# Performance work log

Measured on AMD Instinct MI355X. Metric: run time of the kernel, lower is better.

The kernel has to match this reference:

```python
import jax, jax.numpy as jnp
from jax import lax
import numpy as np

B, IMG, P, CIN, D, DEPTH, H, FF = 32, 512, 16, 4, 256, 4, 8, 2048
N = (IMG // P) ** 2          # 1024 patches
L = N // 2                   # exactly 512 masked patches per batch (static max_len)
DH = D // H
EPS = 1e-5


def layer_norm(x, s, b):
    m = x.mean(-1, keepdims=True)
    v = ((x - m) ** 2).mean(-1, keepdims=True)
    return (x - m) * lax.rsqrt(v + EPS) * s + b


def setup_inputs() -> dict:
    key = jax.random.key(0)
    ks = jax.random.split(key, 16)
    init = lambda k, shp: 0.02 * jax.random.normal(k, shp, jnp.float32)

    image = jax.random.normal(ks[0], (B, 3, IMG, IMG), jnp.float32)
    # patch-granular binary mask: exactly L patches per batch have value 0 (masked)
    scores = jax.random.uniform(ks[1], (B, N))
    idx = jnp.argsort(scores, axis=1)[:, :L]
    pm = jnp.ones((B, N), jnp.float32).at[jnp.arange(B)[:, None], idx].set(0.0)
    mask = jnp.repeat(jnp.repeat(pm.reshape(B, 1, IMG // P, IMG // P), P, 2), P, 3)

    return dict(
        image=image, mask=mask,
        conv_w=init(ks[2], (D, CIN, P, P)), conv_b=jnp.zeros((D,), jnp.float32),
        pos_embed=jax.random.normal(ks[3], (1, N, D), jnp.float32),
        qkv_w=init(ks[4], (DEPTH, D, 3 * D)), qkv_b=jnp.zeros((DEPTH, 3 * D), jnp.float32),
        out_w=init(ks[5], (DEPTH, D, D)), out_b=jnp.zeros((DEPTH, D), jnp.float32),
        ln1_s=jnp.ones((DEPTH, D), jnp.float32), ln1_b=jnp.zeros((DEPTH, D), jnp.float32),
        ff1_w=init(ks[6], (DEPTH, D, FF)), ff1_b=jnp.zeros((DEPTH, FF), jnp.float32),
        ff2_w=init(ks[7], (DEPTH, FF, D)), ff2_b=jnp.zeros((DEPTH, D), jnp.float32),
        ln2_s=jnp.ones((DEPTH, D), jnp.float32), ln2_b=jnp.zeros((DEPTH, D), jnp.float32),
    )


def reference(image, mask, conv_w, conv_b, pos_embed, qkv_w, qkv_b, out_w, out_b,
              ln1_s, ln1_b, ff1_w, ff1_b, ff2_w, ff2_b, ln2_s, ln2_b):
    xin = jnp.concatenate([image, mask], axis=1)                       # [B,4,512,512]
    x = lax.conv_general_dilated(xin, conv_w, (P, P), 'VALID',
                                 dimension_numbers=('NCHW', 'OIHW', 'NCHW'))
    x = x + conv_b[None, :, None, None]                                # [B,D,32,32]
    Bc = x.shape[0]
    x = x.reshape(Bc, D, N).transpose(0, 2, 1)                         # [B,N,D]

    # nearest downsample (factor exactly P): sample at indices i*P
    pmask = mask[:, 0, ::P, ::P].reshape(Bc, N)
    sel = pmask < 0.5                                                  # masked patches
    # stable compaction: indices of masked patches first, in original order
    order = jnp.argsort(jnp.logical_not(sel), axis=1, stable=True)[:, :L]
    tokens = jnp.take_along_axis(x, order[..., None], axis=1)          # [B,L,D]
    pos = pos_embed[0][order]                                          # [B,L,D]
    lengths = sel.sum(axis=1)
    valid = (jnp.arange(L)[None, :] < lengths[:, None])[..., None]
    h = jnp.where(valid, tokens + pos, 0.0)                            # zero padding

    scale = 1.0 / np.sqrt(DH)
    for i in range(DEPTH):  # post-norm torch TransformerEncoderLayer, no dropout
        qkv = h @ qkv_w[i] + qkv_b[i]
        q, k, v = jnp.split(qkv, 3, axis=-1)
        q = q.reshape(Bc, L, H, DH)
        k = k.reshape(Bc, L, H, DH)
        v = v.reshape(Bc, L, H, DH)
        att = jax.nn.softmax(jnp.einsum('bqhd,bkhd->bhqk', q, k) * scale, axis=-1)
        o = jnp.einsum('bhqk,bkhd->bqhd', att, v).reshape(Bc, L, D)
        h = layer_norm(h + o @ out_w[i] + out_b[i], ln1_s[i], ln1_b[i])
        ff = jax.nn.relu(h @ ff1_w[i] + ff1_b[i]) @ ff2_w[i] + ff2_b[i]
        h = layer_norm(h + ff, ln2_s[i], ln2_b[i])
    return h
```

## Files before the change

kernel.cpp:

```cpp
#include <hip/hip_runtime.h>
#include <cstdint>
#include <cstddef>


#define Bq 32
#define Dm 256
#define Lq 512
#define Hh 8
#define FFq 2048
#define Mtok (Bq * Lq)

typedef __attribute__((ext_vector_type(8))) short  short8;
typedef __attribute__((ext_vector_type(4))) float  f32x4;
typedef __attribute__((ext_vector_type(4))) unsigned int u32x4;
typedef __attribute__((ext_vector_type(2))) unsigned int u32x2;

static __device__ __forceinline__ unsigned short f2bf(float f) {
    unsigned int u = __float_as_uint(f);
    unsigned int r = (u + 0x7FFFu + ((u >> 16) & 1u)) >> 16;
    return (unsigned short)r;
}
static __device__ __forceinline__ unsigned int pk2bf(float lo, float hi) {
    return (unsigned int)f2bf(lo) | ((unsigned int)f2bf(hi) << 16);
}

static __device__ __forceinline__ void gload_lds16(const void* g, void* l) {
    __builtin_amdgcn_global_load_lds(
        (const __attribute__((address_space(1))) unsigned int*)g,
        (__attribute__((address_space(3))) unsigned int*)l, 16, 0, 0);
}

static __device__ __forceinline__ int xcd_swz(int id, int grid) {
    return (id & 7) * (grid >> 3) + (id >> 3);
}

__global__ __launch_bounds__(1024) void k_order(const float* __restrict__ mask,
                                                int* __restrict__ order) {
    const int b = blockIdx.x;
    const int n = threadIdx.x;
    const float v = mask[(size_t)b * 262144 + (size_t)(n >> 5) * 8192 + (n & 31) * 16];
    const bool sel = v < 0.5f;
    const unsigned long long ball = __ballot(sel);
    const int wave = n >> 6, lane = n & 63;
    __shared__ int wsum[16];
    __shared__ int wpre[16];
    if (lane == 0) wsum[wave] = __popcll(ball);
    __syncthreads();
    if (n == 0) {
        int s = 0;
        for (int i = 0; i < 16; ++i) { wpre[i] = s; s += wsum[i]; }
    }
    __syncthreads();
    const int rank = wpre[wave] + __popcll(ball & ((1ull << lane) - 1ull));
    if (sel) order[b * Lq + rank] = n;
}

__global__ __launch_bounds__(256) void k_gather(const float* __restrict__ image,
                                                const int* __restrict__ order,
                                                const float* __restrict__ pos,
                                                unsigned short* __restrict__ patchA,
                                                float* __restrict__ posG) {
    __shared__ int pn[16];
    const int tid = threadIdx.x;
    const int tok0 = blockIdx.x * 16;
    if (tid < 16) pn[tid] = order[tok0 + tid];
    __syncthreads();
    const int lane = tid & 63, w4 = tid >> 6;
    const int rr = lane >> 2, col4 = (lane & 3) << 2;
#pragma unroll
    for (int it = 0; it < 12; ++it) {
        const int s = it * 4 + w4;
        const int t = s / 3, cch = s % 3;
        const int n = pn[t];
        const int b = (tok0 + t) >> 9;
        const int pi = n >> 5, pj = n & 31;
        const float4 v = *(const float4*)&image[
            (((size_t)b * 3 + cch) * 512 + pi * 16 + rr) * 512 + pj * 16 + col4];
        unsigned int pk[2] = {pk2bf(v.x, v.y), pk2bf(v.z, v.w)};
        *(uint2*)&patchA[(size_t)(tok0 + t) * 768 + cch * 256 + rr * 16 + col4] =
            *(uint2*)pk;
    }
#pragma unroll
    for (int it = 0; it < 4; ++it) {
        const int t = it * 4 + w4;
        *(float4*)&posG[(size_t)(tok0 + t) * Dm + lane * 4] =
            *(const float4*)&pos[(size_t)pn[t] * Dm + lane * 4];
    }
}

__global__ __launch_bounds__(256) void k_wprep_all(const float* __restrict__ qkv_w,
                                                   const float* __restrict__ out_w,
                                                   const float* __restrict__ ff1_w,
                                                   const float* __restrict__ ff2_w,
                                                   const float* __restrict__ conv_w,
                                                   unsigned short* __restrict__ Wq,
                                                   unsigned short* __restrict__ Wo,
                                                   unsigned short* __restrict__ Wf1,
                                                   unsigned short* __restrict__ Wf2,
                                                   unsigned short* __restrict__ We) {
    int idx = blockIdx.x;
    if (idx >= 1280) {
        const int i = (idx - 1280) * 256 + threadIdx.x;
        const int d = i / 96, k8 = (i % 96) * 8;
        const float4 a = *(const float4*)&conv_w[(size_t)d * 1024 + k8];
        const float4 b = *(const float4*)&conv_w[(size_t)d * 1024 + k8 + 4];
        unsigned int pk[4] = {pk2bf(a.x, a.y), pk2bf(a.z, a.w),
                              pk2bf(b.x, b.y), pk2bf(b.z, b.w)};
        *(uint4*)&We[(size_t)d * 768 + k8] = *(uint4*)pk;
        return;
    }
    __shared__ float tile[64][65];
    const float* W; unsigned short* WT; int K, N, l, r;
    if (idx < 192)      { l = idx / 48;          r = idx % 48;  K = 256;  N = 768;  W = qkv_w; WT = Wq; }
    else if (idx < 256) { l = (idx - 192) / 16;  r = idx & 15;  K = 256;  N = 256;  W = out_w; WT = Wo; }
    else if (idx < 768) { l = (idx - 256) / 128; r = (idx - 256) % 128; K = 256;  N = 2048; W = ff1_w; WT = Wf1; }
    else                { l = (idx - 768) / 128; r = (idx - 768) % 128; K = 2048; N = 256;  W = ff2_w; WT = Wf2; }
    const int nTiles = N >> 6;
    const int n0 = (r % nTiles) * 64, k0 = (r / nTiles) * 64;
    W  += (size_t)l * K * N;
    WT += (size_t)l * K * N;
    const int t = threadIdx.x;
#pragma unroll
    for (int it = 0; it < 4; ++it) {
        const int rr = (t >> 4) + it * 16, c4 = (t & 15) * 4;
        *(float4*)&tile[rr][c4] = *(const float4*)&W[(size_t)(k0 + rr) * N + n0 + c4];
    }
    __syncthreads();
    const int n = t & 63, kq = t >> 6;
    unsigned short pk[16];
#pragma unroll
    for (int j = 0; j < 16; ++j) pk[j] = f2bf(tile[kq * 16 + j][n]);
    unsigned short* dst = &WT[(size_t)(n0 + n) * K + k0 + kq * 16];
    *(uint4*)dst       = *(uint4*)&pk[0];
    *(uint4*)(dst + 8) = *(uint4*)&pk[8];
}

template <bool RELU, bool RES, bool OUT32, bool OUT16, int NBUF, bool SWZ>
__global__ __launch_bounds__(256) void k_mgemm(const unsigned short* __restrict__ A,
                                               const unsigned short* __restrict__ W,
                                               const float* __restrict__ bias,
                                               const float* __restrict__ R,
                                               float* __restrict__ C32,
                                               unsigned short* __restrict__ C16,
                                               int ntiles, int M, int N, int K) {
    __shared__ unsigned short Al[128 * 64 * NBUF];
    __shared__ unsigned short Bl[128 * 64 * NBUF];
    const int tid = threadIdx.x;
    const int lane = tid & 63, wave = tid >> 6;
    const int wm = wave >> 1, wn = wave & 1;
    int id = blockIdx.x;
    if constexpr (SWZ) id = xcd_swz(id, (int)gridDim.x);
    const int n0 = (id % ntiles) * 128, m0 = (id / ntiles) * 128;
    const int c = lane >> 4, a15 = lane & 15;
    f32x4 acc[4][4] = {};

    const int srow = lane >> 3;
    const int sgran = (lane & 7) ^ srow;
    const int KT = K >> 6;

    auto stage = [&](int buf, int kt) {
        const int k0 = kt << 6;
#pragma unroll
        for (int q = 0; q < 4; ++q) {
            const int rbase = wave * 32 + q * 8;
            gload_lds16(A + (size_t)(m0 + rbase + srow) * K + k0 + sgran * 8,
                        &Al[buf * 8192 + rbase * 64]);
            gload_lds16(W + (size_t)(n0 + rbase + srow) * K + k0 + sgran * 8,
                        &Bl[buf * 8192 + rbase * 64]);
        }
    };
    auto compute = [&](int buf) {
        const int bo = buf * 8192;
#pragma unroll
        for (int kc = 0; kc < 2; ++kc) {
            short8 af[4], bf[4];
#pragma unroll
            for (int fm = 0; fm < 4; ++fm) {
                const int row = wm * 64 + fm * 16 + a15;
                const int slot = (kc * 4 + c) ^ (row & 7);
                af[fm] = *(const short8*)&Al[bo + row * 64 + slot * 8];
            }
#pragma unroll
            for (int fn = 0; fn < 4; ++fn) {
                const int row = wn * 64 + fn * 16 + a15;
                const int slot = (kc * 4 + c) ^ (row & 7);
                bf[fn] = *(const short8*)&Bl[bo + row * 64 + slot * 8];
            }
#pragma unroll
            for (int fm = 0; fm < 4; ++fm)
#pragma unroll
                for (int fn = 0; fn < 4; ++fn)
                    acc[fm][fn] = __builtin_amdgcn_mfma_f32_16x16x32_bf16(
                        af[fm], bf[fn], acc[fm][fn], 0, 0, 0);
        }
    };

    if constexpr (NBUF == 2) {
        stage(0, 0);
        for (int kt = 0; kt < KT; ++kt) {
            const int cur = kt & 1;
            if (kt + 1 < KT) {
                stage(cur ^ 1, kt + 1);
                asm volatile("s_waitcnt vmcnt(8)" ::: "memory");
            } else {
                asm volatile("s_waitcnt vmcnt(0)" ::: "memory");
            }
            __builtin_amdgcn_s_barrier();
            compute(cur);
            __builtin_amdgcn_s_barrier();
        }
    } else {
        for (int kt = 0; kt < KT; ++kt) {
            __syncthreads();
            stage(0, kt);
            __syncthreads();
            compute(0);
        }
    }
#pragma unroll
    for (int fn = 0; fn < 4; ++fn) {
        const int col = n0 + wn * 64 + fn * 16 + a15;
        const float bv = bias[col];
#pragma unroll
        for (int fm = 0; fm < 4; ++fm) {
            const int mrow = m0 + wm * 64 + fm * 16 + c * 4;
#pragma unroll
            for (int r = 0; r < 4; ++r) {
                float v = acc[fm][fn][r] + bv;
                if constexpr (RES) v += R[(size_t)(mrow + r) * N + col];
                if constexpr (RELU) v = fmaxf(v, 0.f);
                if constexpr (OUT32) C32[(size_t)(mrow + r) * N + col] = v;
                if constexpr (OUT16) C16[(size_t)(mrow + r) * N + col] = f2bf(v);
            }
        }
    }
}

template <bool RELU, bool OUT16>
__global__ __launch_bounds__(512) void k_mgemm8(const unsigned short* __restrict__ A,
                                                const unsigned short* __restrict__ W,
                                                const float* __restrict__ bias,
                                                unsigned short* __restrict__ C16,
                                                int ntiles, int N, int K) {
    __shared__ unsigned short Al[256 * 64];
    __shared__ unsigned short Bl[128 * 64];
    const int tid = threadIdx.x;
    const int lane = tid & 63, wave = tid >> 6;
    const int wm = wave >> 1, wn = wave & 1;
    const int id = xcd_swz((int)blockIdx.x, (int)gridDim.x);
    const int n0 = (id % ntiles) * 128, m0 = (id / ntiles) * 256;
    const int c = lane >> 4, a15 = lane & 15;
    f32x4 acc[4][4] = {};

    const int srow = lane >> 3;
    const int sgran = (lane & 7) ^ srow;
    const int KT = K >> 6;

    for (int kt = 0; kt < KT; ++kt) {
        const int k0 = kt << 6;
        __syncthreads();
#pragma unroll
        for (int q = 0; q < 4; ++q) {
            const int rbase = wave * 32 + q * 8;
            gload_lds16(A + (size_t)(m0 + rbase + srow) * K + k0 + sgran * 8,
                        &Al[rbase * 64]);
        }
#pragma unroll
        for (int q = 0; q < 2; ++q) {
            const int rbase = wave * 16 + q * 8;
            gload_lds16(W + (size_t)(n0 + rbase + srow) * K + k0 + sgran * 8,
                        &Bl[rbase * 64]);
        }
        __syncthreads();
#pragma unroll
        for (int kc = 0; kc < 2; ++kc) {
            short8 af[4], bf[4];
#pragma unroll
            for (int fm = 0; fm < 4; ++fm) {
                const int row = wm * 64 + fm * 16 + a15;
                const int slot = (kc * 4 + c) ^ (row & 7);
                af[fm] = *(const short8*)&Al[row * 64 + slot * 8];
            }
#pragma unroll
            for (int fn = 0; fn < 4; ++fn) {
                const int row = wn * 64 + fn * 16 + a15;
                const int slot = (kc * 4 + c) ^ (row & 7);
                bf[fn] = *(const short8*)&Bl[row * 64 + slot * 8];
            }
#pragma unroll
            for (int fm = 0; fm < 4; ++fm)
#pragma unroll
                for (int fn = 0; fn < 4; ++fn)
                    acc[fm][fn] = __builtin_amdgcn_mfma_f32_16x16x32_bf16(
                        af[fm], bf[fn], acc[fm][fn], 0, 0, 0);
        }
    }
#pragma unroll
    for (int fn = 0; fn < 4; ++fn) {
        const int col = n0 + wn * 64 + fn * 16 + a15;
        const float bv = bias[col];
#pragma unroll
        for (int fm = 0; fm < 4; ++fm) {
            const int mrow = m0 + wm * 64 + fm * 16 + c * 4;
#pragma unroll
            for (int r = 0; r < 4; ++r) {
                float v = acc[fm][fn][r] + bv;
                if constexpr (RELU) v = fmaxf(v, 0.f);
                if constexpr (OUT16) C16[(size_t)(mrow + r) * N + col] = f2bf(v);
            }
        }
    }
}

__global__ __launch_bounds__(256) void k_gemm_ln(const unsigned short* __restrict__ A,
                                                 const unsigned short* __restrict__ W,
                                                 const float* __restrict__ bias,
                                                 const float* __restrict__ R,
                                                 const float* __restrict__ lns,
                                                 const float* __restrict__ lnb,
                                                 float* __restrict__ Y32,
                                                 unsigned short* __restrict__ Y16,
                                                 int K) {
    __shared__ unsigned short Al[32 * 64 * 2];
    __shared__ unsigned short Bl[256 * 64 * 2];
    __shared__ float redS[4][32];
    __shared__ float redQ[4][32];
    const int tid = threadIdx.x;
    const int lane = tid & 63, wave = tid >> 6;
    const int m0 = xcd_swz((int)blockIdx.x, (int)gridDim.x) * 32;
    const int c = lane >> 4, a15 = lane & 15;
    f32x4 acc[2][4] = {};

    const int srow = lane >> 3;
    const int sgran = (lane & 7) ^ srow;
    const int KT = K >> 6;

    auto stage = [&](int buf, int kt) {
        const int k0 = kt << 6;
        gload_lds16(A + (size_t)(m0 + wave * 8 + srow) * K + k0 + sgran * 8,
                    &Al[buf * 2048 + (wave * 8) * 64]);
#pragma unroll
        for (int q = 0; q < 8; ++q) {
            const int rbase = wave * 64 + q * 8;
            gload_lds16(W + (size_t)(rbase + srow) * K + k0 + sgran * 8,
                        &Bl[buf * 16384 + rbase * 64]);
        }
    };
    auto compute = [&](int buf) {
        const int ao = buf * 2048, bo = buf * 16384;
#pragma unroll
        for (int kc = 0; kc < 2; ++kc) {
            short8 af[2], bf[4];
#pragma unroll
            for (int fm = 0; fm < 2; ++fm) {
                const int row = fm * 16 + a15;
                const int slot = (kc * 4 + c) ^ (row & 7);
                af[fm] = *(const short8*)&Al[ao + row * 64 + slot * 8];
            }
#pragma unroll
            for (int fn = 0; fn < 4; ++fn) {
                const int row = wave * 64 + fn * 16 + a15;
                const int slot = (kc * 4 + c) ^ (row & 7);
                bf[fn] = *(const short8*)&Bl[bo + row * 64 + slot * 8];
            }
#pragma unroll
            for (int fm = 0; fm < 2; ++fm)
#pragma unroll
                for (int fn = 0; fn < 4; ++fn)
                    acc[fm][fn] = __builtin_amdgcn_mfma_f32_16x16x32_bf16(
                        af[fm], bf[fn], acc[fm][fn], 0, 0, 0);
        }
    };

    stage(0, 0);
    for (int kt = 0; kt < KT; ++kt) {
        const int cur = kt & 1;
        if (kt + 1 < KT) {
            stage(cur ^ 1, kt + 1);
            asm volatile("s_waitcnt vmcnt(9)" ::: "memory");
        } else {
            asm volatile("s_waitcnt vmcnt(0)" ::: "memory");
        }
        __builtin_amdgcn_s_barrier();
        compute(cur);
        __builtin_amdgcn_s_barrier();
    }

    float bv[4], sg[4], bg[4];
#pragma unroll
    for (int fn = 0; fn < 4; ++fn) {
        const int col = wave * 64 + fn * 16 + a15;
        bv[fn] = bias[col]; sg[fn] = lns[col]; bg[fn] = lnb[col];
    }
#pragma unroll
    for (int fm = 0; fm < 2; ++fm) {
        const int mrow = m0 + fm * 16 + c * 4;
#pragma unroll
        for (int r = 0; r < 4; ++r) {
            float ps = 0.f, pq = 0.f;
#pragma unroll
            for (int fn = 0; fn < 4; ++fn) {
                const int col = wave * 64 + fn * 16 + a15;
                float v = acc[fm][fn][r] + bv[fn] + R[(size_t)(mrow + r) * Dm + col];
                acc[fm][fn][r] = v;
                ps += v; pq += v * v;
            }
#pragma unroll
            for (int off = 1; off < 16; off <<= 1) {
                ps += __shfl_xor(ps, off);
                pq += __shfl_xor(pq, off);
            }
            if (a15 == 0) {
                redS[wave][fm * 16 + c * 4 + r] = ps;
                redQ[wave][fm * 16 + c * 4 + r] = pq;
            }
        }
    }
    __syncthreads();
#pragma unroll
    for (int fm = 0; fm < 2; ++fm) {
        const int lrow = fm * 16 + c * 4;
        const int mrow = m0 + lrow;
#pragma unroll
        for (int r = 0; r < 4; ++r) {
            const float totS = redS[0][lrow + r] + redS[1][lrow + r] +
                               redS[2][lrow + r] + redS[3][lrow + r];
            const float totQ = redQ[0][lrow + r] + redQ[1][lrow + r] +
                               redQ[2][lrow + r] + redQ[3][lrow + r];
            const float mean = totS * (1.f / 256.f);
            const float var = totQ * (1.f / 256.f) - mean * mean;
            const float inv = rsqrtf(var + 1e-5f);
#pragma unroll
            for (int fn = 0; fn < 4; ++fn) {
                const int col = wave * 64 + fn * 16 + a15;
                const float y = (acc[fm][fn][r] - mean) * inv * sg[fn] + bg[fn];
                Y32[(size_t)(mrow + r) * Dm + col] = y;
                Y16[(size_t)(mrow + r) * Dm + col] = f2bf(y);
            }
        }
    }
}

__global__ __launch_bounds__(512) void k_attn(const unsigned short* __restrict__ QKV,
                                              unsigned short* __restrict__ O) {
    __shared__ unsigned short Kl[512 * 32];
    __shared__ unsigned short Vt[32 * 512];
    const int bh = xcd_swz((int)blockIdx.x, (int)gridDim.x);
    const int b = bh >> 3, h = bh & 7;
    const int tid = threadIdx.x, lane = tid & 63, wave = tid >> 6;
    const int c = lane >> 4, a15 = lane & 15;
    const size_t qkvbase = (size_t)b * Lq * 768 + h * 32;

    {
        const int srow = lane >> 2;
        const int sg = (lane & 3) ^ ((srow >> 1) & 3);
#pragma unroll
        for (int q = 0; q < 4; ++q) {
            const int rbase = wave * 64 + q * 16;
            gload_lds16(QKV + qkvbase + (size_t)(rbase + srow) * 768 + 256 + sg * 8,
                        &Kl[rbase * 32]);
        }
    }
    {
        const int kg = tid & 127, dg = tid >> 7;
        u32x4 v[4];
#pragma unroll
        for (int kk = 0; kk < 4; ++kk)
            v[kk] = *(const u32x4*)&QKV[qkvbase + (size_t)(kg * 4 + kk) * 768 + 512 + dg * 8];
#pragma unroll
        for (int dd = 0; dd < 8; ++dd) {
            const int d = dg * 8 + dd;
            unsigned short e[4];
#pragma unroll
            for (int kk = 0; kk < 4; ++kk) {
                const unsigned int word = v[kk][dd >> 1];
                e[kk] = (dd & 1) ? (unsigned short)(word >> 16) : (unsigned short)(word & 0xffff);
            }
            unsigned int pk[2];
            pk[0] = (unsigned int)e[0] | ((unsigned int)e[1] << 16);
            pk[1] = (unsigned int)e[2] | ((unsigned int)e[3] << 16);
            *(uint2*)&Vt[d * 512 + ((kg ^ (d & 7)) << 2)] = *(uint2*)pk;
        }
    }
    const int q0w = wave * 64;
    short8 qf[4];
#pragma unroll
    for (int fn = 0; fn < 4; ++fn)
        qf[fn] = *(const short8*)&QKV[qkvbase + (size_t)(q0w + fn * 16 + a15) * 768 + c * 8];
    __syncthreads();

    const float scale = 0.17677669529663687f;
    f32x4 oacc[2][4] = {};
    float mstat[4], lstat[4];
#pragma unroll
    for (int fn = 0; fn < 4; ++fn) { mstat[fn] = -1e30f; lstat[fn] = 0.f; }
    const f32x4 zero4 = {0.f, 0.f, 0.f, 0.f};

    for (int t = 0; t < 16; ++t) {
        const int kv0 = t * 32;
        short8 kf[2];
#pragma unroll
        for (int fm = 0; fm < 2; ++fm) {
            const int row = kv0 + fm * 16 + a15;
            const int slot = c ^ ((row >> 1) & 3);
            kf[fm] = *(const short8*)&Kl[row * 32 + slot * 8];
        }
        short8 vf[2];
#pragma unroll
        for (int fmd = 0; fmd < 2; ++fmd) {
            const int d = fmd * 16 + a15;
            const int g0 = (t * 8 + c) ^ (d & 7);
            const int g1 = (t * 8 + 4 + c) ^ (d & 7);
            const u32x2 r0 = *(const u32x2*)&Vt[d * 512 + g0 * 4];
            const u32x2 r1 = *(const u32x2*)&Vt[d * 512 + g1 * 4];
            const u32x4 cmb = {r0[0], r0[1], r1[0], r1[1]};
            vf[fmd] = __builtin_bit_cast(short8, cmb);
        }
        f32x4 s[2][4];
#pragma unroll
        for (int fm = 0; fm < 2; ++fm)
#pragma unroll
            for (int fn = 0; fn < 4; ++fn)
                s[fm][fn] = __builtin_amdgcn_mfma_f32_16x16x32_bf16(kf[fm], qf[fn], zero4, 0, 0, 0);
#pragma unroll
        for (int fn = 0; fn < 4; ++fn) {
            float p[8];
            float tmax = -1e30f;
#pragma unroll
            for (int fm = 0; fm < 2; ++fm)
#pragma unroll
                for (int r = 0; r < 4; ++r) {
                    const float x = s[fm][fn][r] * scale;
                    p[fm * 4 + r] = x;
                    tmax = fmaxf(tmax, x);
                }
            tmax = fmaxf(tmax, __shfl_xor(tmax, 16));
            tmax = fmaxf(tmax, __shfl_xor(tmax, 32));
            const float mnew = fmaxf(mstat[fn], tmax);
            const float alpha = __expf(mstat[fn] - mnew);
            mstat[fn] = mnew;
            float tsum = 0.f;
            short8 pf;
#pragma unroll
            for (int j = 0; j < 8; ++j) {
                const float e = __expf(p[j] - mnew);
                tsum += e;
                pf[j] = (short)f2bf(e);
            }
            tsum += __shfl_xor(tsum, 16);
            tsum += __shfl_xor(tsum, 32);
            lstat[fn] = lstat[fn] * alpha + tsum;
#pragma unroll
            for (int fmd = 0; fmd < 2; ++fmd) {
                oacc[fmd][fn] *= alpha;
                oacc[fmd][fn] = __builtin_amdgcn_mfma_f32_16x16x32_bf16(
                    vf[fmd], pf, oacc[fmd][fn], 0, 0, 0);
            }
        }
    }
#pragma unroll
    for (int fn = 0; fn < 4; ++fn) {
        const float invl = 1.f / lstat[fn];
        const size_t qrow = (size_t)(b * Lq + q0w + fn * 16 + a15);
#pragma unroll
        for (int fmd = 0; fmd < 2; ++fmd)
#pragma unroll
            for (int r = 0; r < 4; ++r)
                O[qrow * Dm + h * 32 + fmd * 16 + c * 4 + r] = f2bf(oacc[fmd][fn][r] * invl);
    }
}

extern "C" void kernel_launch(void* const* d_in, const int* in_sizes, int n_in,
                              void* d_out, int out_size, void* d_ws, size_t ws_size,
                              hipStream_t stream) {
    const float* image  = (const float*)d_in[0];
    const float* mask   = (const float*)d_in[1];
    const float* conv_w = (const float*)d_in[2];
    const float* conv_b = (const float*)d_in[3];
    const float* pos    = (const float*)d_in[4];
    const float* qkv_w  = (const float*)d_in[5];
    const float* qkv_b  = (const float*)d_in[6];
    const float* out_w  = (const float*)d_in[7];
    const float* out_b  = (const float*)d_in[8];
    const float* ln1_s  = (const float*)d_in[9];
    const float* ln1_b  = (const float*)d_in[10];
    const float* ff1_w  = (const float*)d_in[11];
    const float* ff1_b  = (const float*)d_in[12];
    const float* ff2_w  = (const float*)d_in[13];
    const float* ff2_b  = (const float*)d_in[14];
    const float* ln2_s  = (const float*)d_in[15];
    const float* ln2_b  = (const float*)d_in[16];
    float* out = (float*)d_out;

    char* w = (char*)d_ws;
    int* order            = (int*)w;            w += 64 * 1024;
    float* H32            = (float*)w;          w += (size_t)Mtok * Dm * 4;
    unsigned short* H16   = (unsigned short*)w; w += (size_t)Mtok * Dm * 2;
    unsigned short* QKV16 = (unsigned short*)w; w += (size_t)Mtok * 768 * 2;
    unsigned short* O16   = (unsigned short*)w; w += (size_t)Mtok * Dm * 2;
    unsigned short* F16   = (unsigned short*)w; w += (size_t)Mtok * FFq * 2;
    unsigned short* Wq    = (unsigned short*)w; w += (size_t)4 * 768 * 256 * 2;
    unsigned short* Wo    = (unsigned short*)w; w += (size_t)4 * 256 * 256 * 2;
    unsigned short* Wf1   = (unsigned short*)w; w += (size_t)4 * 2048 * 256 * 2;
    unsigned short* Wf2   = (unsigned short*)w; w += (size_t)4 * 256 * 2048 * 2;
    unsigned short* We    = (unsigned short*)w; w += (size_t)256 * 768 * 2;
    unsigned short* patchA = F16;
    float* posG            = (float*)(F16 + (size_t)Mtok * 768);

    k_order<<<Bq, 1024, 0, stream>>>(mask, order);
    k_gather<<<Mtok / 16, 256, 0, stream>>>(image, order, pos, patchA, posG);
    k_wprep_all<<<1376, 256, 0, stream>>>(qkv_w, out_w, ff1_w, ff2_w, conv_w,
                                          Wq, Wo, Wf1, Wf2, We);

    k_mgemm<false, true, true, true, 2, true><<<256, 256, 0, stream>>>(
        patchA, We, conv_b, posG, H32, H16, 2, Mtok, 256, 768);

    for (int i = 0; i < 4; ++i) {
        k_mgemm8<false, true><<<384, 512, 0, stream>>>(
            H16, Wq + (size_t)i * 768 * 256, qkv_b + (size_t)i * 768,
            QKV16, 6, 768, 256);
        k_attn<<<Bq * Hh, 512, 0, stream>>>(QKV16, O16);
        k_gemm_ln<<<Mtok / 32, 256, 0, stream>>>(
            O16, Wo + (size_t)i * 256 * 256, out_b + (size_t)i * 256, H32,
            ln1_s + i * Dm, ln1_b + i * Dm, H32, H16, 256);
        k_mgemm8<true, true><<<1024, 512, 0, stream>>>(
            H16, Wf1 + (size_t)i * 2048 * 256, ff1_b + (size_t)i * FFq,
            F16, 16, 2048, 256);
        float* dst32 = (i == 3) ? out : H32;
        k_gemm_ln<<<Mtok / 32, 256, 0, stream>>>(
            F16, Wf2 + (size_t)i * 256 * 2048, ff2_b + (size_t)i * 256, H32,
            ln2_s + i * Dm, ln2_b + i * Dm, dst32, H16, 2048);
    }
    (void)in_sizes; (void)n_in; (void)out_size; (void)ws_size;
}
```

Baseline: 549.3 us.

## Split FF2 GEMM+LayerNorm into large-tile GEMM and separate LN kernel

Replaces the fused FF2 GEMM+LayerNorm (32-row blocks) with the 256x128-tile k_mgemm8, now extended with residual add and fp32 output, followed by a standalone row LayerNorm kernel. The aim is better weight reuse and MFMA efficiency for the K=2048 GEMM. In exchange it writes and rereads an fp32 intermediate buffer, and the GEMM launches only 128 blocks, which may underfill the GPU.

```diff
diff --git a/kernel.cpp b/kernel.cpp
--- a/kernel.cpp
+++ b/kernel.cpp
@@ -236,10 +236,12 @@
     }
 }
 
-template <bool RELU, bool OUT16>
+template <bool RELU, bool RES, bool OUT32, bool OUT16>
 __global__ __launch_bounds__(512) void k_mgemm8(const unsigned short* __restrict__ A,
                                                 const unsigned short* __restrict__ W,
                                                 const float* __restrict__ bias,
+                                                const float* __restrict__ R,
+                                                float* __restrict__ C32,
                                                 unsigned short* __restrict__ C16,
                                                 int ntiles, int N, int K) {
     __shared__ unsigned short Al[256 * 64];
@@ -305,11 +307,42 @@
 #pragma unroll
             for (int r = 0; r < 4; ++r) {
                 float v = acc[fm][fn][r] + bv;
+                if constexpr (RES) v += R[(size_t)(mrow + r) * N + col];
                 if constexpr (RELU) v = fmaxf(v, 0.f);
+                if constexpr (OUT32) C32[(size_t)(mrow + r) * N + col] = v;
                 if constexpr (OUT16) C16[(size_t)(mrow + r) * N + col] = f2bf(v);
             }
         }
     }
+}
+
+__global__ __launch_bounds__(256) void k_ln(const float* __restrict__ X,
+                                            float* __restrict__ Y32,
+                                            unsigned short* __restrict__ Y16,
+                                            const float* __restrict__ s,
+                                            const float* __restrict__ b) {
+    const int row = blockIdx.x * 4 + (threadIdx.x >> 6);
+    const int lane = threadIdx.x & 63;
+    const float4 v = *(const float4*)&X[(size_t)row * Dm + lane * 4];
+    float sum = v.x + v.y + v.z + v.w;
+#pragma unroll
+    for (int off = 32; off; off >>= 1) sum += __shfl_xor(sum, off);
+    const float mean = sum * (1.f / 256.f);
+    const float dx[4] = {v.x - mean, v.y - mean, v.z - mean, v.w - mean};
+    float vv = dx[0] * dx[0] + dx[1] * dx[1] + dx[2] * dx[2] + dx[3] * dx[3];
+#pragma unroll
+    for (int off = 32; off; off >>= 1) vv += __shfl_xor(vv, off);
+    const float inv = rsqrtf(vv * (1.f / 256.f) + 1e-5f);
+    const float4 sv = *(const float4*)&s[lane * 4];
+    const float4 bv = *(const float4*)&b[lane * 4];
+    float o[4];
+    o[0] = dx[0] * inv * sv.x + bv.x;
+    o[1] = dx[1] * inv * sv.y + bv.y;
+    o[2] = dx[2] * inv * sv.z + bv.z;
+    o[3] = dx[3] * inv * sv.w + bv.w;
+    *(float4*)&Y32[(size_t)row * Dm + lane * 4] = *(float4*)o;
+    unsigned int pk[2] = {pk2bf(o[0], o[1]), pk2bf(o[2], o[3])};
+    *(uint2*)&Y16[(size_t)row * Dm + lane * 4] = *(uint2*)pk;
 }
 
 __global__ __launch_bounds__(256) void k_gemm_ln(const unsigned short* __restrict__ A,
@@ -598,6 +631,7 @@
     unsigned short* H16   = (unsigned short*)w; w += (size_t)Mtok * Dm * 2;
     unsigned short* QKV16 = (unsigned short*)w; w += (size_t)Mtok * 768 * 2;
     unsigned short* O16   = (unsigned short*)w; w += (size_t)Mtok * Dm * 2;
+    float* X32            = (float*)w;          w += (size_t)Mtok * Dm * 4;
     unsigned short* F16   = (unsigned short*)w; w += (size_t)Mtok * FFq * 2;
     unsigned short* Wq    = (unsigned short*)w; w += (size_t)4 * 768 * 256 * 2;
     unsigned short* Wo    = (unsigned short*)w; w += (size_t)4 * 256 * 256 * 2;
@@ -616,20 +650,22 @@
         patchA, We, conv_b, posG, H32, H16, 2, Mtok, 256, 768);
 
     for (int i = 0; i < 4; ++i) {
-        k_mgemm8<false, true><<<384, 512, 0, stream>>>(
+        k_mgemm8<false, false, false, true><<<384, 512, 0, stream>>>(
             H16, Wq + (size_t)i * 768 * 256, qkv_b + (size_t)i * 768,
-            QKV16, 6, 768, 256);
+            nullptr, nullptr, QKV16, 6, 768, 256);
         k_attn<<<Bq * Hh, 512, 0, stream>>>(QKV16, O16);
         k_gemm_ln<<<Mtok / 32, 256, 0, stream>>>(
             O16, Wo + (size_t)i * 256 * 256, out_b + (size_t)i * 256, H32,
             ln1_s + i * Dm, ln1_b + i * Dm, H32, H16, 256);
-        k_mgemm8<true, true><<<1024, 512, 0, stream>>>(
+        k_mgemm8<true, false, false, true><<<1024, 512, 0, stream>>>(
             H16, Wf1 + (size_t)i * 2048 * 256, ff1_b + (size_t)i * FFq,
-            F16, 16, 2048, 256);
+            nullptr, nullptr, F16, 16, 2048, 256);
+        k_mgemm8<false, true, true, false><<<128, 512, 0, stream>>>(
+            F16, Wf2 + (size_t)i * 256 * 2048, ff2_b + (size_t)i * 256,
+            H32, X32, nullptr, 2, 256, 2048);
         float* dst32 = (i == 3) ? out : H32;
-        k_gemm_ln<<<Mtok / 32, 256, 0, stream>>>(
-            F16, Wf2 + (size_t)i * 256 * 2048, ff2_b + (size_t)i * 256, H32,
-            ln2_s + i * Dm, ln2_b + i * Dm, dst32, H16, 2048);
+        k_ln<<<Mtok / 4, 256, 0, stream>>>(X32, dst32, H16,
+                                           ln2_s + i * Dm, ln2_b + i * Dm);
     }
     (void)in_sizes; (void)n_in; (void)out_size; (void)ws_size;
 }
```

New measurement: 657.5 us. +19.7%, slower.
